# Performance work log

Hardware: AMD Instinct MI355X
Metric: run time of the kernel (lower is better)

## Reference

```python
import jax, jax.numpy as jnp
import numpy as np

B, CN, CL, E, H, FF = 2, 16, 128, 1024, 16, 4096
HD = E // H
EPS = 1e-5


def _layernorm(x, g, b):
    m = jnp.mean(x, axis=-1, keepdims=True)
    v = jnp.mean((x - m) ** 2, axis=-1, keepdims=True)
    return (x - m) * jax.lax.rsqrt(v + EPS) * g + b


def _self_attention(v, Wv, Wk, Wq, Wo, bo):
    # v: [N, chunk_num, chunk_len, E] -> flatten chunks to seq len L
    N = v.shape[0]
    L = v.shape[1] * v.shape[2]
    x = v.reshape(N, L, H, HD)
    q = x @ Wq          # per-head head_dim x head_dim projections (shared across heads)
    k = x @ Wk
    val = x @ Wv
    energy = jnp.einsum('nqhd,nkhd->nhqk', q, k)
    att = jax.nn.softmax(energy / np.float32(np.sqrt(E)), axis=-1)  # note: scaled by sqrt(embed_size), as in source
    out = jnp.einsum('nhqk,nkhd->nqhd', att, val).reshape(N, L, E)
    return out @ Wo + bo


def setup_inputs() -> dict:
    key0 = jax.random.key(0)
    ks = jax.random.split(key0, 14)
    s_hd = np.float32(1.0 / np.sqrt(HD))
    s_e = np.float32(1.0 / np.sqrt(E))
    s_ff = np.float32(1.0 / np.sqrt(FF))
    return {
        'value': jax.random.normal(ks[0], (B, CN, 2, CL, E), jnp.float32),
        'key': jnp.zeros((1,), jnp.float32),
        'query': jax.random.normal(ks[1], (B, CN, CL, E), jnp.float32),
        'mask': jnp.zeros((1,), jnp.int32),
        'retrieved_passages': jnp.zeros((1,), jnp.int32),
        'Wv': jax.random.normal(ks[2], (HD, HD), jnp.float32) * s_hd,
        'Wk': jax.random.normal(ks[3], (HD, HD), jnp.float32) * s_hd,
        'Wq': jax.random.normal(ks[4], (HD, HD), jnp.float32) * s_hd,
        'Wo': jax.random.normal(ks[5], (E, E), jnp.float32) * s_e,
        'bo': jnp.zeros((E,), jnp.float32),
        'g1': jnp.ones((E,), jnp.float32),
        'b1': jnp.zeros((E,), jnp.float32),
        'W1': jax.random.normal(ks[6], (E, FF), jnp.float32) * s_e,
        'bf1': jnp.zeros((FF,), jnp.float32),
        'W2': jax.random.normal(ks[7], (FF, E), jnp.float32) * s_ff,
        'bf2': jnp.zeros((E,), jnp.float32),
        'g3': jnp.ones((E,), jnp.float32),
        'b3': jnp.zeros((E,), jnp.float32),
    }


def reference(value, key, query, mask, retrieved_passages,
              Wv, Wk, Wq, Wo, bo, g1, b1, W1, bf1, W2, bf2, g3, b3):
    # key, mask, retrieved_passages are unused by the original module's forward
    Bq, cn, cl, _ = query.shape
    v1 = value[:, :, 0, :, :]   # [B, CN, CL, E]
    v2 = value[:, :, 1, :, :]
    sa1 = _self_attention(v1, Wv, Wk, Wq, Wo, bo)
    sa2 = _self_attention(v2, Wv, Wk, Wq, Wo, bo)
    sa = (sa1 + sa2).reshape(Bq, cn, cl, -1)
    x = _layernorm(sa + query, g1, b1)           # dropout p=0 -> identity
    f = jax.nn.relu(x @ W1 + bf1) @ W2 + bf2
    return _layernorm(f + x, g3, b3)
```

## Files before the change

kernel.cpp:

```cpp
#include <hip/hip_runtime.h>
#include <hip/hip_bf16.h>

typedef __bf16 bf16_t;
typedef __attribute__((ext_vector_type(8))) __bf16 bf16x8;
typedef __attribute__((ext_vector_type(4))) __bf16 bf16x4;
typedef __attribute__((ext_vector_type(4))) float f32x4;
typedef __attribute__((ext_vector_type(16))) float f32x16;

#define DEV __device__ __forceinline__
#define LOG2E 1.44269504088896f

DEV void gload16(const bf16_t* g, void* l) {
  __builtin_amdgcn_global_load_lds((const __attribute__((address_space(1))) void*)g,
                                   (__attribute__((address_space(3))) void*)l, 16, 0, 0);
}

DEV f32x4 mfma16(bf16x8 a, bf16x8 b, f32x4 c) {
  return __builtin_amdgcn_mfma_f32_16x16x32_bf16(a, b, c, 0, 0, 0);
}
DEV f32x16 mfma32(bf16x8 a, bf16x8 b, f32x16 c) {
  return __builtin_amdgcn_mfma_f32_32x32x16_bf16(a, b, c, 0, 0, 0);
}

DEV float fexp2(float x) {
#if __has_builtin(__builtin_amdgcn_exp2f)
  return __builtin_amdgcn_exp2f(x);
#else
  float r;
  asm("v_exp_f32 %0, %1" : "=v"(r) : "v"(x));
  return r;
#endif
}

DEV bf16x8 cvt8(const float* p0, const float* p1) {
  bf16x8 v;
  v[0] = (bf16_t)p0[0]; v[1] = (bf16_t)p0[1]; v[2] = (bf16_t)p0[2]; v[3] = (bf16_t)p0[3];
  v[4] = (bf16_t)p1[0]; v[5] = (bf16_t)p1[1]; v[6] = (bf16_t)p1[2]; v[7] = (bf16_t)p1[3];
  return v;
}

DEV unsigned pk2(float lo, float hi) {
  union { bf16_t h[2]; unsigned u; } x;
  x.h[0] = (bf16_t)lo; x.h[1] = (bf16_t)hi;
  return x.u;
}

DEV bf16x8 lds_read_swz7(const bf16_t* base, int row, int kByte) {
  int off = (row << 7) + (kByte ^ ((row & 7) << 4));
  return *(const bf16x8*)((const char*)base + off);
}
DEV bf16x8 lds_read_swz8b(const bf16_t* base, int row, int kByte) {
  int off = (row << 8) + (kByte ^ ((row & 15) << 4));
  return *(const bf16x8*)((const char*)base + off);
}

DEV void wconv_tile(const float* in, bf16_t* out, int R, int C, int tile) {
  __shared__ alignas(16) bf16_t Ts[64][72];
  int tilesC = C >> 6;
  int tr = tile / tilesC, tc = tile % tilesC;
  int t = threadIdx.x;
  int rr = t >> 3, c0 = (t & 7) << 3;
#pragma unroll
  for (int i = 0; i < 2; ++i) {
    int row = rr + i * 32;
    const float* src = in + (size_t)(tr * 64 + row) * C + tc * 64 + c0;
    float4 a = *(const float4*)src;
    float4 b = *(const float4*)(src + 4);
    *(bf16x8*)&Ts[row][c0] = cvt8(&a.x, &b.x);
  }
  __syncthreads();
#pragma unroll
  for (int i = 0; i < 2; ++i) {
    int nl = rr + i * 32;
    bf16x8 v;
#pragma unroll
    for (int j = 0; j < 8; ++j) v[j] = Ts[c0 + j][nl];
    *(bf16x8*)(out + (size_t)(tc * 64 + nl) * R + tr * 64 + c0) = v;
  }
}

__global__ __launch_bounds__(256) void k_wconv3(const float* __restrict__ Wo,
    const float* __restrict__ W1, const float* __restrict__ W2,
    bf16_t* __restrict__ WoT, bf16_t* __restrict__ W1T, bf16_t* __restrict__ W2T) {
  int b = blockIdx.x;
  if (b < 256) wconv_tile(Wo, WoT, 1024, 1024, b);
  else if (b < 1280) wconv_tile(W1, W1T, 1024, 4096, b - 256);
  else wconv_tile(W2, W2T, 4096, 1024, b - 1280);
}

__global__ __launch_bounds__(256) void k_qkv(const float* __restrict__ value,
    const float* __restrict__ Wq, const float* __restrict__ Wk, const float* __restrict__ Wv,
    bf16_t* __restrict__ Q, bf16_t* __restrict__ K, bf16_t* __restrict__ VT) {
  __shared__ alignas(16) bf16_t Xs[128 * 72];
  __shared__ alignas(16) bf16_t Wt[3][64 * 72];
  int b = blockIdx.x;
  int cn = b & 15, h = (b >> 4) & 15, n = (b >> 8) & 1, s = b >> 9;
  int t = threadIdx.x, lane = t & 63, w = t >> 6;
  int lg = (lane >> 4) & 3, ll = lane & 15;
  int hbase = (s * 2 + n) * 16 + h;
  const float* xbase = value + (size_t)(((n * 16 + cn) * 2 + s) * 128) * 1024 + h * 64;
#pragma unroll
  for (int i = 0; i < 4; ++i) {
    int c = t + i * 256;
    int row = c >> 3, d0 = (c & 7) << 3;
    const float* src = xbase + (size_t)row * 1024 + d0;
    float4 a = *(const float4*)src;
    float4 b2 = *(const float4*)(src + 4);
    *(bf16x8*)&Xs[row * 72 + d0] = cvt8(&a.x, &b2.x);
  }
  const float* Wm[3] = {Wq, Wk, Wv};
#pragma unroll
  for (int m = 0; m < 3; ++m) {
    float sc = (m == 0) ? (0.03125f * LOG2E) : 1.0f;
    for (int i = 0; i < 16; ++i) {
      int f = t * 16 + i;
      int k = f >> 6, col = f & 63;
      Wt[m][col * 72 + k] = (bf16_t)(Wm[m][f] * sc);
    }
  }
  __syncthreads();
  f32x4 acc[3][2][4] = {};
#pragma unroll
  for (int kc = 0; kc < 2; ++kc) {
    bf16x8 a[2];
#pragma unroll
    for (int rt = 0; rt < 2; ++rt)
      a[rt] = *(const bf16x8*)&Xs[(w * 32 + rt * 16 + ll) * 72 + kc * 32 + lg * 8];
#pragma unroll
    for (int m = 0; m < 3; ++m)
#pragma unroll
      for (int ct = 0; ct < 4; ++ct) {
        bf16x8 bf = *(const bf16x8*)&Wt[m][(ct * 16 + ll) * 72 + kc * 32 + lg * 8];
#pragma unroll
        for (int rt = 0; rt < 2; ++rt)
          acc[m][rt][ct] = mfma16(a[rt], bf, acc[m][rt][ct]);
      }
  }
  bf16_t* outp[2] = {Q, K};
  size_t obase = ((size_t)hbase * 2048 + cn * 128) * 64;
#pragma unroll
  for (int m = 0; m < 2; ++m)
#pragma unroll
    for (int rt = 0; rt < 2; ++rt)
#pragma unroll
      for (int ct = 0; ct < 4; ++ct)
#pragma unroll
        for (int r = 0; r < 4; ++r) {
          int lrow = w * 32 + rt * 16 + lg * 4 + r;
          int d = ct * 16 + ll;
          outp[m][obase + (size_t)lrow * 64 + d] = (bf16_t)acc[m][rt][ct][r];
        }
  __syncthreads();
  bf16_t* XsT = Xs;
#pragma unroll
  for (int rt = 0; rt < 2; ++rt)
#pragma unroll
    for (int ct = 0; ct < 4; ++ct)
#pragma unroll
      for (int r = 0; r < 4; ++r) {
        int lrow = w * 32 + rt * 16 + lg * 4 + r;
        int d = ct * 16 + ll;
        XsT[d * 136 + lrow] = (bf16_t)acc[2][rt][ct][r];
      }
  __syncthreads();
#pragma unroll
  for (int p = 0; p < 4; ++p) {
    int d = p * 16 + (t >> 4);
    int l0 = (t & 15) * 8;
    bf16x8 v;
#pragma unroll
    for (int j = 0; j < 8; ++j) {
      int pos = l0 + j;
      int key = (pos & ~12) | ((pos & 4) << 1) | ((pos & 8) >> 1);
      v[j] = XsT[d * 136 + key];
    }
    *(bf16x8*)(VT + ((size_t)hbase * 64 + d) * 2048 + cn * 128 + l0) = v;
  }
}

__global__ __launch_bounds__(256, 4) void k_flash(const bf16_t* __restrict__ Qg,
    const bf16_t* __restrict__ Kg, const bf16_t* __restrict__ VTg, bf16_t* __restrict__ AO) {
  __shared__ alignas(16) bf16_t Ks[2][128 * 64];
  __shared__ alignas(16) bf16_t Vt[2][64 * 128];
  int b0 = blockIdx.x;
  int b = (b0 & 7) * 128 + (b0 >> 3);
  int qt = b & 15, h = (b >> 4) & 15, n = (b >> 8) & 1, s = b >> 9;
  int t = threadIdx.x, lane = t & 63, w = t >> 6;
  int l31 = lane & 31, hi = lane >> 5;
  size_t hoff = ((size_t)((s * 2 + n) * 16 + h)) << 17;
  const bf16_t* Qh = Qg + hoff;
  const bf16_t* Kh = Kg + hoff;
  const bf16_t* VTh = VTg + hoff;
  int qrow = qt * 128 + w * 32 + l31;
  bf16x8 qf[4];
#pragma unroll
  for (int kc4 = 0; kc4 < 4; ++kc4)
    qf[kc4] = *(const bf16x8*)(Qh + (size_t)qrow * 64 + kc4 * 16 + hi * 8);
  f32x16 oacc[2], lacc, zro;
#pragma unroll
  for (int r = 0; r < 16; ++r) {
    oacc[0][r] = 0.f; oacc[1][r] = 0.f; lacc[r] = 0.f; zro[r] = 0.f;
  }
  bf16x8 ones;
#pragma unroll
  for (int j = 0; j < 8; ++j) ones[j] = (bf16_t)1.0f;

  int l8s = (((lane & 7) ^ (lane >> 3)) << 3);
  const bf16_t* kbase = Kh + (size_t)(w * 32 + (lane >> 3)) * 64 + l8s;
  const bf16_t* vbase[4];
#pragma unroll
  for (int i = 0; i < 4; ++i) {
    int row = w * 16 + i * 4 + (lane >> 4);
    vbase[i] = VTh + (size_t)row * 2048 + (((lane & 15) ^ (row & 15)) << 3);
  }
  auto stage = [&](int buf, int kt0) {
    int koff = kt0 * 8192;
    int voff = kt0 * 128;
#pragma unroll
    for (int i = 0; i < 4; ++i)
      gload16(kbase + koff + i * 512, (char*)Ks[buf] + (w * 4 + i) * 1024);
#pragma unroll
    for (int i = 0; i < 4; ++i)
      gload16(vbase[i] + voff, (char*)Vt[buf] + (w * 4 + i) * 1024);
  };

  stage(0, 0);
  __syncthreads();
  for (int kt0 = 0; kt0 < 16; ++kt0) {
    int cur = kt0 & 1;
    if (kt0 < 15) stage(cur ^ 1, kt0 + 1);
    f32x16 sacc[4];
    __builtin_amdgcn_s_setprio(1);
#pragma unroll
    for (int kb = 0; kb < 4; ++kb) {
      bf16x8 kf = lds_read_swz7(Ks[cur], kb * 32 + l31, hi * 16);
      sacc[kb] = mfma32(kf, qf[0], zro);
#pragma unroll
      for (int kc4 = 1; kc4 < 4; ++kc4) {
        kf = lds_read_swz7(Ks[cur], kb * 32 + l31, kc4 * 32 + hi * 16);
        sacc[kb] = mfma32(kf, qf[kc4], sacc[kb]);
      }
    }
    __builtin_amdgcn_s_setprio(0);
#pragma unroll
    for (int kb = 0; kb < 4; ++kb) {
#pragma unroll
      for (int r = 0; r < 16; ++r)
        sacc[kb][r] = fexp2(sacc[kb][r]);
      __builtin_amdgcn_s_setprio(1);
#pragma unroll
      for (int c = 0; c < 2; ++c) {
        int base = 8 * c;
        union { unsigned u[4]; bf16x8 v; } pb;
#pragma unroll
        for (int jj = 0; jj < 4; ++jj)
          pb.u[jj] = pk2(sacc[kb][base + 2 * jj], sacc[kb][base + 2 * jj + 1]);
        int kc16 = kb * 2 + c;
        lacc = mfma32(ones, pb.v, lacc);
#pragma unroll
        for (int dblk = 0; dblk < 2; ++dblk) {
          bf16x8 vf = lds_read_swz8b(Vt[cur], dblk * 32 + l31, kc16 * 32 + hi * 16);
          oacc[dblk] = mfma32(vf, pb.v, oacc[dblk]);
        }
      }
      __builtin_amdgcn_s_setprio(0);
    }
    __syncthreads();
  }
  float lrun = lacc[0];
  bf16_t* AOs = AO + ((size_t)s) * 4194304;
  float rl = 1.f / lrun;
  size_t rowbase = ((size_t)(n * 2048 + qrow)) * 1024 + h * 64;
#pragma unroll
  for (int dblk = 0; dblk < 2; ++dblk)
#pragma unroll
    for (int rp = 0; rp < 4; ++rp) {
      bf16x4 ov;
#pragma unroll
      for (int rq = 0; rq < 4; ++rq) ov[rq] = (bf16_t)(oacc[dblk][rp * 4 + rq] * rl);
      int d0 = dblk * 32 + rp * 8 + hi * 4;
      *(bf16x4*)(AOs + rowbase + d0) = ov;
    }
}

__global__ __launch_bounds__(256) void k_sum(const bf16_t* __restrict__ a,
    const bf16_t* __restrict__ b, bf16_t* __restrict__ o) {
  int i = (blockIdx.x * 256 + threadIdx.x) * 8;
  bf16x8 va = *(const bf16x8*)(a + i);
  bf16x8 vb = *(const bf16x8*)(b + i);
  bf16x8 vo;
#pragma unroll
  for (int j = 0; j < 8; ++j) vo[j] = (bf16_t)((float)va[j] + (float)vb[j]);
  *(bf16x8*)(o + i) = vo;
}

template <int EPI>
__global__ __launch_bounds__(256) void k_gemm(const bf16_t* __restrict__ A,
    const bf16_t* __restrict__ BT, void* __restrict__ outp,
    const float* __restrict__ bias, const void* __restrict__ add,
    int M, int N, int K) {
  __shared__ alignas(16) bf16_t As[128 * 64];
  __shared__ alignas(16) bf16_t Bs[128 * 64];
  int ntn = N >> 7;
  int nwg = gridDim.x;
  int b0 = blockIdx.x;
  int cpx = nwg >> 3;
  int b = (b0 & 7) * cpx + (b0 >> 3);
  int ks = 0, k0 = 0, kend = K;
  if (EPI == 3) {
    int half = nwg >> 1;
    ks = (b >= half) ? 1 : 0;
    b -= ks * half;
    int kh = K >> 1;
    k0 = ks * kh;
    kend = k0 + kh;
  }
  int bm = b / ntn, bn = b % ntn;
  int t = threadIdx.x, lane = t & 63, w = t >> 6;
  int wr = w >> 1, wc = w & 1;
  int lg = (lane >> 4) & 3, ll = lane & 15;
  f32x4 acc[4][4] = {};
  int rA = bm * 128, rB = bn * 128;
  int l8s = (((lane & 7) ^ (lane >> 3)) << 3);
  for (int kt = k0; kt < kend; kt += 64) {
#pragma unroll
    for (int i = 0; i < 4; ++i) {
      int kb = w * 4 + i;
      int row = kb * 8 + (lane >> 3);
      gload16(A + (size_t)(rA + row) * K + kt + l8s, (char*)As + kb * 1024);
      gload16(BT + (size_t)(rB + row) * K + kt + l8s, (char*)Bs + kb * 1024);
    }
    __syncthreads();
#pragma unroll
    for (int kc = 0; kc < 2; ++kc) {
      bf16x8 a[4], bb[4];
#pragma unroll
      for (int m = 0; m < 4; ++m)
        a[m] = lds_read_swz7(As, wr * 64 + m * 16 + ll, kc * 64 + lg * 16);
#pragma unroll
      for (int nn = 0; nn < 4; ++nn)
        bb[nn] = lds_read_swz7(Bs, wc * 64 + nn * 16 + ll, kc * 64 + lg * 16);
#pragma unroll
      for (int m = 0; m < 4; ++m)
#pragma unroll
        for (int nn = 0; nn < 4; ++nn)
          acc[m][nn] = mfma16(a[m], bb[nn], acc[m][nn]);
    }
    __syncthreads();
  }
#pragma unroll
  for (int m = 0; m < 4; ++m)
#pragma unroll
    for (int nn = 0; nn < 4; ++nn)
#pragma unroll
      for (int r = 0; r < 4; ++r) {
        int row = bm * 128 + wr * 64 + m * 16 + lg * 4 + r;
        int col = bn * 128 + wc * 64 + nn * 16 + ll;
        float v = acc[m][nn][r];
        size_t idx = (size_t)row * N + col;
        if (EPI == 0) {
          v += 2.f * bias[col] + ((const float*)add)[idx];
          ((float*)outp)[idx] = v;
        } else if (EPI == 1) {
          v += bias[col];
          ((bf16_t*)outp)[idx] = (bf16_t)fmaxf(v, 0.f);
        } else {
          float* dst = ks ? (float*)add : (float*)outp;
          dst[idx] = v;
        }
      }
}

template <int MODE>
__global__ __launch_bounds__(256) void k_ln(const float* __restrict__ T,
    const float* __restrict__ g, const float* __restrict__ b,
    float* __restrict__ xf, bf16_t* __restrict__ xb,
    const float* __restrict__ T2, const float* __restrict__ bias2,
    const float* __restrict__ add2) {
  int row = blockIdx.x, t = threadIdx.x;
  float4 v = ((const float4*)(T + (size_t)row * 1024))[t];
  if (MODE == 2) {
    const float4 v2 = ((const float4*)(T2 + (size_t)row * 1024))[t];
    const float4 vb = ((const float4*)bias2)[t];
    const float4 va = ((const float4*)(add2 + (size_t)row * 1024))[t];
    v.x += v2.x + vb.x + va.x;
    v.y += v2.y + vb.y + va.y;
    v.z += v2.z + vb.z + va.z;
    v.w += v2.w + vb.w + va.w;
  }
  float s1 = v.x + v.y + v.z + v.w;
  float s2 = v.x * v.x + v.y * v.y + v.z * v.z + v.w * v.w;
#pragma unroll
  for (int off = 1; off < 64; off <<= 1) {
    s1 += __shfl_xor(s1, off);
    s2 += __shfl_xor(s2, off);
  }
  __shared__ float red[8];
  int w = t >> 6, lane = t & 63;
  if (lane == 0) { red[w] = s1; red[w + 4] = s2; }
  __syncthreads();
  s1 = red[0] + red[1] + red[2] + red[3];
  s2 = red[4] + red[5] + red[6] + red[7];
  float mean = s1 * (1.f / 1024.f);
  float var = s2 * (1.f / 1024.f) - mean * mean;
  float rstd = rsqrtf(var + 1e-5f);
  const float4 gv = ((const float4*)g)[t];
  const float4 bv = ((const float4*)b)[t];
  float4 o;
  o.x = (v.x - mean) * rstd * gv.x + bv.x;
  o.y = (v.y - mean) * rstd * gv.y + bv.y;
  o.z = (v.z - mean) * rstd * gv.z + bv.z;
  o.w = (v.w - mean) * rstd * gv.w + bv.w;
  ((float4*)(xf + (size_t)row * 1024))[t] = o;
  if (MODE == 0) {
    bf16x4 ob;
    ob[0] = (bf16_t)o.x; ob[1] = (bf16_t)o.y; ob[2] = (bf16_t)o.z; ob[3] = (bf16_t)o.w;
    *(bf16x4*)(xb + (size_t)row * 1024 + t * 4) = ob;
  }
}

extern "C" void kernel_launch(void* const* d_in, const int* in_sizes, int n_in,
                              void* d_out, int out_size, void* d_ws, size_t ws_size,
                              hipStream_t stream) {
  const float* value = (const float*)d_in[0];
  const float* query = (const float*)d_in[2];
  const float* Wv = (const float*)d_in[5];
  const float* Wk = (const float*)d_in[6];
  const float* Wq = (const float*)d_in[7];
  const float* Wo = (const float*)d_in[8];
  const float* bo = (const float*)d_in[9];
  const float* g1 = (const float*)d_in[10];
  const float* b1 = (const float*)d_in[11];
  const float* W1 = (const float*)d_in[12];
  const float* bf1 = (const float*)d_in[13];
  const float* W2 = (const float*)d_in[14];
  const float* bf2 = (const float*)d_in[15];
  const float* g3 = (const float*)d_in[16];
  const float* b3 = (const float*)d_in[17];

  char* ws = (char*)d_ws;
  bf16_t* Qb    = (bf16_t*)(ws + 0x0000000);
  bf16_t* Kb    = (bf16_t*)(ws + 0x1000000);
  bf16_t* VTb   = (bf16_t*)(ws + 0x2000000);
  bf16_t* AO    = (bf16_t*)(ws + 0x3000000);
  bf16_t* AOsum = (bf16_t*)(ws + 0x0000000);
  float*  T1    = (float*) (ws + 0x1000000);
  float*  Xf    = (float*) (ws + 0x2000000);
  bf16_t* Xb    = (bf16_t*)(ws + 0x0000000);
  bf16_t* Hb    = (bf16_t*)(ws + 0x3000000);
  float*  Psk0  = (float*) (ws + 0x0000000);
  float*  Psk1  = (float*) (ws + 0x1000000);
  bf16_t* WoT   = (bf16_t*)(ws + 0x5000000);
  bf16_t* W1T   = (bf16_t*)(ws + 0x5200000);
  bf16_t* W2T   = (bf16_t*)(ws + 0x5A00000);

  k_wconv3<<<2304, 256, 0, stream>>>(Wo, W1, W2, WoT, W1T, W2T);
  k_qkv<<<1024, 256, 0, stream>>>(value, Wq, Wk, Wv, Qb, Kb, VTb);
  k_flash<<<1024, 256, 0, stream>>>(Qb, Kb, VTb, AO);
  k_sum<<<2048, 256, 0, stream>>>(AO, AO + 4194304, AOsum);
  k_gemm<0><<<256, 256, 0, stream>>>(AOsum, WoT, T1, bo, query, 4096, 1024, 1024);
  k_ln<0><<<4096, 256, 0, stream>>>(T1, g1, b1, Xf, Xb, nullptr, nullptr, nullptr);
  k_gemm<1><<<1024, 256, 0, stream>>>(Xb, W1T, Hb, bf1, nullptr, 4096, 4096, 1024);
  k_gemm<3><<<512, 256, 0, stream>>>(Hb, W2T, Psk0, nullptr, Psk1, 4096, 1024, 4096);
  k_ln<2><<<4096, 256, 0, stream>>>(Psk0, g3, b3, (float*)d_out, nullptr,
                                    Psk1, bf2, Xf);
}
```

Measured before the change: 262.3 us.

## Merge weight conversion into QKV kernel and split-K the Wo GEMM

Combines the weight-transpose conversion and the QKV projection into one launch, with a shared LDS pool and branching on block index. This removes one kernel launch and lets the two independent jobs overlap on the GPU. The Wo projection GEMM now uses the split-K mode (512 blocks writing two partial buffers), and the first layernorm sums the partials, bias and query residual. This gives the 4096x1024x1024 GEMM more blocks to fill the GPU, at the cost of extra fp32 partial traffic and a larger LDS footprint for the weight-conversion blocks.

```diff
diff --git a/kernel.cpp b/kernel.cpp
--- a/kernel.cpp
+++ b/kernel.cpp
@@ -54,8 +54,8 @@
   return *(const bf16x8*)((const char*)base + off);
 }
 
-DEV void wconv_tile(const float* in, bf16_t* out, int R, int C, int tile) {
-  __shared__ alignas(16) bf16_t Ts[64][72];
+DEV void wconv_tile(bf16_t* pool, const float* in, bf16_t* out, int R, int C, int tile) {
+  bf16_t (*Ts)[72] = (bf16_t(*)[72])pool;
   int tilesC = C >> 6;
   int tr = tile / tilesC, tc = tile % tilesC;
   int t = threadIdx.x;
@@ -79,21 +79,11 @@
   }
 }
 
-__global__ __launch_bounds__(256) void k_wconv3(const float* __restrict__ Wo,
-    const float* __restrict__ W1, const float* __restrict__ W2,
-    bf16_t* __restrict__ WoT, bf16_t* __restrict__ W1T, bf16_t* __restrict__ W2T) {
-  int b = blockIdx.x;
-  if (b < 256) wconv_tile(Wo, WoT, 1024, 1024, b);
-  else if (b < 1280) wconv_tile(W1, W1T, 1024, 4096, b - 256);
-  else wconv_tile(W2, W2T, 4096, 1024, b - 1280);
-}
-
-__global__ __launch_bounds__(256) void k_qkv(const float* __restrict__ value,
-    const float* __restrict__ Wq, const float* __restrict__ Wk, const float* __restrict__ Wv,
-    bf16_t* __restrict__ Q, bf16_t* __restrict__ K, bf16_t* __restrict__ VT) {
-  __shared__ alignas(16) bf16_t Xs[128 * 72];
-  __shared__ alignas(16) bf16_t Wt[3][64 * 72];
-  int b = blockIdx.x;
+DEV void qkv_body(bf16_t* pool, int b, const float* value,
+    const float* Wq, const float* Wk, const float* Wv,
+    bf16_t* Q, bf16_t* K, bf16_t* VT) {
+  bf16_t* Xs = pool;
+  bf16_t* Wt = pool + 128 * 72;
   int cn = b & 15, h = (b >> 4) & 15, n = (b >> 8) & 1, s = b >> 9;
   int t = threadIdx.x, lane = t & 63, w = t >> 6;
   int lg = (lane >> 4) & 3, ll = lane & 15;
@@ -115,7 +105,7 @@
     for (int i = 0; i < 16; ++i) {
       int f = t * 16 + i;
       int k = f >> 6, col = f & 63;
-      Wt[m][col * 72 + k] = (bf16_t)(Wm[m][f] * sc);
+      Wt[m * 64 * 72 + col * 72 + k] = (bf16_t)(Wm[m][f] * sc);
     }
   }
   __syncthreads();
@@ -130,7 +120,7 @@
     for (int m = 0; m < 3; ++m)
 #pragma unroll
       for (int ct = 0; ct < 4; ++ct) {
-        bf16x8 bf = *(const bf16x8*)&Wt[m][(ct * 16 + ll) * 72 + kc * 32 + lg * 8];
+        bf16x8 bf = *(const bf16x8*)&Wt[m * 64 * 72 + (ct * 16 + ll) * 72 + kc * 32 + lg * 8];
 #pragma unroll
         for (int rt = 0; rt < 2; ++rt)
           acc[m][rt][ct] = mfma16(a[rt], bf, acc[m][rt][ct]);
@@ -175,6 +165,23 @@
       v[j] = XsT[d * 136 + key];
     }
     *(bf16x8*)(VT + ((size_t)hbase * 64 + d) * 2048 + cn * 128 + l0) = v;
+  }
+}
+
+__global__ __launch_bounds__(256) void k_prep(const float* __restrict__ value,
+    const float* __restrict__ Wq, const float* __restrict__ Wk, const float* __restrict__ Wv,
+    bf16_t* __restrict__ Q, bf16_t* __restrict__ K, bf16_t* __restrict__ VT,
+    const float* __restrict__ Wo, const float* __restrict__ W1, const float* __restrict__ W2,
+    bf16_t* __restrict__ WoT, bf16_t* __restrict__ W1T, bf16_t* __restrict__ W2T) {
+  __shared__ alignas(16) bf16_t pool[128 * 72 + 3 * 64 * 72];
+  int b = blockIdx.x;
+  if (b < 1024) {
+    qkv_body(pool, b, value, Wq, Wk, Wv, Q, K, VT);
+  } else {
+    int tile = b - 1024;
+    if (tile < 256) wconv_tile(pool, Wo, WoT, 1024, 1024, tile);
+    else if (tile < 1280) wconv_tile(pool, W1, W1T, 1024, 4096, tile - 256);
+    else wconv_tile(pool, W2, W2T, 4096, 1024, tile - 1280);
   }
 }
 
@@ -358,10 +365,7 @@
         int col = bn * 128 + wc * 64 + nn * 16 + ll;
         float v = acc[m][nn][r];
         size_t idx = (size_t)row * N + col;
-        if (EPI == 0) {
-          v += 2.f * bias[col] + ((const float*)add)[idx];
-          ((float*)outp)[idx] = v;
-        } else if (EPI == 1) {
+        if (EPI == 1) {
           v += bias[col];
           ((bf16_t*)outp)[idx] = (bf16_t)fmaxf(v, 0.f);
         } else {
@@ -379,14 +383,15 @@
     const float* __restrict__ add2) {
   int row = blockIdx.x, t = threadIdx.x;
   float4 v = ((const float4*)(T + (size_t)row * 1024))[t];
-  if (MODE == 2) {
+  {
     const float4 v2 = ((const float4*)(T2 + (size_t)row * 1024))[t];
     const float4 vb = ((const float4*)bias2)[t];
     const float4 va = ((const float4*)(add2 + (size_t)row * 1024))[t];
-    v.x += v2.x + vb.x + va.x;
-    v.y += v2.y + vb.y + va.y;
-    v.z += v2.z + vb.z + va.z;
-    v.w += v2.w + vb.w + va.w;
+    float bs = (MODE == 3) ? 2.f : 1.f;
+    v.x += v2.x + bs * vb.x + va.x;
+    v.y += v2.y + bs * vb.y + va.y;
+    v.z += v2.z + bs * vb.z + va.z;
+    v.w += v2.w + bs * vb.w + va.w;
   }
   float s1 = v.x + v.y + v.z + v.w;
   float s2 = v.x * v.x + v.y * v.y + v.z * v.z + v.w * v.w;
@@ -412,7 +417,7 @@
   o.z = (v.z - mean) * rstd * gv.z + bv.z;
   o.w = (v.w - mean) * rstd * gv.w + bv.w;
   ((float4*)(xf + (size_t)row * 1024))[t] = o;
-  if (MODE == 0) {
+  if (MODE == 3) {
     bf16x4 ob;
     ob[0] = (bf16_t)o.x; ob[1] = (bf16_t)o.y; ob[2] = (bf16_t)o.z; ob[3] = (bf16_t)o.w;
     *(bf16x4*)(xb + (size_t)row * 1024 + t * 4) = ob;
@@ -444,7 +449,8 @@
   bf16_t* VTb   = (bf16_t*)(ws + 0x2000000);
   bf16_t* AO    = (bf16_t*)(ws + 0x3000000);
   bf16_t* AOsum = (bf16_t*)(ws + 0x0000000);
-  float*  T1    = (float*) (ws + 0x1000000);
+  float*  Pg0   = (float*) (ws + 0x1000000);
+  float*  Pg1   = (float*) (ws + 0x3000000);
   float*  Xf    = (float*) (ws + 0x2000000);
   bf16_t* Xb    = (bf16_t*)(ws + 0x0000000);
   bf16_t* Hb    = (bf16_t*)(ws + 0x3000000);
@@ -454,12 +460,12 @@
   bf16_t* W1T   = (bf16_t*)(ws + 0x5200000);
   bf16_t* W2T   = (bf16_t*)(ws + 0x5A00000);
 
-  k_wconv3<<<2304, 256, 0, stream>>>(Wo, W1, W2, WoT, W1T, W2T);
-  k_qkv<<<1024, 256, 0, stream>>>(value, Wq, Wk, Wv, Qb, Kb, VTb);
+  k_prep<<<3328, 256, 0, stream>>>(value, Wq, Wk, Wv, Qb, Kb, VTb,
+                                   Wo, W1, W2, WoT, W1T, W2T);
   k_flash<<<1024, 256, 0, stream>>>(Qb, Kb, VTb, AO);
   k_sum<<<2048, 256, 0, stream>>>(AO, AO + 4194304, AOsum);
-  k_gemm<0><<<256, 256, 0, stream>>>(AOsum, WoT, T1, bo, query, 4096, 1024, 1024);
-  k_ln<0><<<4096, 256, 0, stream>>>(T1, g1, b1, Xf, Xb, nullptr, nullptr, nullptr);
+  k_gemm<3><<<512, 256, 0, stream>>>(AOsum, WoT, Pg0, nullptr, Pg1, 4096, 1024, 1024);
+  k_ln<3><<<4096, 256, 0, stream>>>(Pg0, g1, b1, Xf, Xb, Pg1, bo, query);
   k_gemm<1><<<1024, 256, 0, stream>>>(Xb, W1T, Hb, bf1, nullptr, 4096, 4096, 1024);
   k_gemm<3><<<512, 256, 0, stream>>>(Hb, W2T, Psk0, nullptr, Psk1, 4096, 1024, 4096);
   k_ln<2><<<4096, 256, 0, stream>>>(Psk0, g3, b3, (float*)d_out, nullptr,
```

Result: no change. 260.6 us (-0.7%).
